# Performance work log

Measured on AMD Instinct MI355X. Metric: run time of the kernel, lower is better.

The kernel has to match this reference:

```python
import jax, jax.numpy as jnp
import numpy as np

B, T, A_DIM, Z_DIM, K = 128, 80, 32, 64, 16


def setup_inputs() -> dict:
    key = jax.random.key(0)
    k1, k2, k3, k4 = jax.random.split(key, 4)
    obs = jax.random.normal(k1, (B, T, A_DIM), jnp.float32)
    alpha_logits = jax.random.normal(k2, (B, T, K), jnp.float32)
    # torch init: A = eye(z) repeated K times; small noise keeps 80-step recursion stable
    A_K = jnp.eye(Z_DIM, dtype=jnp.float32)[None] + 0.005 * jax.random.normal(k3, (K, Z_DIM, Z_DIM), jnp.float32)
    # torch init: C = 0.05 * randn
    C_K = 0.05 * jax.random.normal(k4, (K, A_DIM, Z_DIM), jnp.float32)
    return {"obs": obs, "alpha_logits": alpha_logits, "A_K": A_K, "C_K": C_K}


def _kalman(obs, A, C):
    # obs [B,T,a], A [B,T,z,z], C [B,T,a,z]
    Bq, Tq, a_dim = obs.shape
    z_dim = A.shape[-1]
    dt = obs.dtype
    Q = 0.08 * jnp.eye(z_dim, dtype=dt)
    R = 0.03 * jnp.eye(a_dim, dtype=dt)
    I = jnp.eye(z_dim, dtype=dt)

    obs_t = jnp.swapaxes(obs, 0, 1)          # [T,B,a]
    A_t = jnp.swapaxes(A, 0, 1)              # [T,B,z,z]
    C_t = jnp.swapaxes(C, 0, 1)              # [T,B,a,z]
    A_next = jnp.concatenate([A_t[1:], A_t[-1:]], axis=0)  # A[t+1]; last unused

    mu0 = jnp.zeros((Bq, z_dim), dt)
    sig0 = jnp.broadcast_to(20.0 * I, (Bq, z_dim, z_dim))

    def filt_step(carry, inp):
        mu_p, sig_p, mu_prev = carry
        At, Anx, Ct, y = inp
        CtT = jnp.swapaxes(Ct, -1, -2)
        S = Ct @ sig_p @ CtT + R                       # [B,a,a]
        Kg = sig_p @ CtT @ jnp.linalg.inv(S)            # [B,z,a]
        Amu = jnp.einsum('bij,bj->bi', At, mu_prev)     # A_t mu_{t-1}
        err = y - jnp.einsum('bij,bj->bi', Ct, Amu)
        mu_f = Amu + jnp.einsum('bij,bj->bi', Kg, err)
        sig_f = (I - Kg @ Ct) @ sig_p
        mu_pn = jnp.einsum('bij,bj->bi', Anx, mu_f)     # prediction with A_{t+1}
        sig_pn = Anx @ sig_f @ jnp.swapaxes(Anx, -1, -2) + Q
        return (mu_pn, sig_pn, mu_f), (mu_f, sig_f, mu_p, sig_p)

    _, (mu_f, sig_f, mu_p, sig_p) = jax.lax.scan(
        filt_step, (mu0, sig0, mu0), (A_t, A_next, C_t, obs_t))

    def smooth_step(carry, inp):
        mu_s, sig_s = carry
        mf, sf, Anx, mpn, spn = inp
        J = sf @ jnp.swapaxes(Anx, -1, -2) @ jnp.linalg.inv(spn)
        mu = mf + jnp.einsum('bij,bj->bi', J, mu_s - mpn)
        sig = sf + J @ (sig_s - spn) @ jnp.swapaxes(J, -1, -2)
        return (mu, sig), (mu, sig)

    init = (mu_f[-1], sig_f[-1])
    _, (mu_sm, sig_sm) = jax.lax.scan(
        smooth_step, init,
        (mu_f[:-1], sig_f[:-1], A_t[1:], mu_p[1:], sig_p[1:]),
        reverse=True)
    mu_sm = jnp.concatenate([mu_sm, mu_f[-1:]], axis=0)
    sig_sm = jnp.concatenate([sig_sm, sig_f[-1:]], axis=0)
    return jnp.swapaxes(mu_sm, 0, 1), jnp.swapaxes(sig_sm, 0, 1)  # [B,T,z], [B,T,z,z]


def reference(obs, alpha_logits, A_K, C_K):
    w = jax.nn.softmax(alpha_logits, axis=-1)                # [B,T,K]
    A = jnp.einsum('btk,kij->btij', w, A_K)                  # [B,T,z,z]
    C = jnp.einsum('btk,kij->btij', w, C_K)                  # [B,T,a,z]
    return _kalman(obs, A, C)
```

## Files before the change

kernel.cpp:

```cpp
#include <hip/hip_runtime.h>

#define B_ 128
#define T_ 80
#define AD 32
#define ZD 64
#define KD 16
#define S8 68
#define SC 36

__device__ __forceinline__ float4 ld4(const float* p) { return *(const float4*)p; }
__device__ __forceinline__ void st4f(float* p, float4 v) { *(float4*)p = v; }

__device__ __forceinline__ float4 comb4(float4 c, float4 x0, float4 x1, float4 x2, float4 x3) {
    return make_float4(c.x*x0.x + c.y*x1.x + c.z*x2.x + c.w*x3.x,
                       c.x*x0.y + c.y*x1.y + c.z*x2.y + c.w*x3.y,
                       c.x*x0.z + c.y*x1.z + c.z*x2.z + c.w*x3.z,
                       c.x*x0.w + c.y*x1.w + c.z*x2.w + c.w*x3.w);
}

__device__ __forceinline__ void pinv4(float4 q0, float4 q1, float4 q2, float4 q3,
                                      float4& pi0, float4& pi1, float4& pi2, float4& pi3)
{
    const float ra = 1.0f / (q0.x*q1.y - q0.y*q1.x);
    const float ai00 =  q1.y*ra, ai01 = -q0.y*ra, ai10 = -q1.x*ra, ai11 = q0.x*ra;
    const float ca00 = q2.x*ai00 + q2.y*ai10, ca01 = q2.x*ai01 + q2.y*ai11;
    const float ca10 = q3.x*ai00 + q3.y*ai10, ca11 = q3.x*ai01 + q3.y*ai11;
    const float s00 = q2.z - (ca00*q0.z + ca01*q1.z), s01 = q2.w - (ca00*q0.w + ca01*q1.w);
    const float s10 = q3.z - (ca10*q0.z + ca11*q1.z), s11 = q3.w - (ca10*q0.w + ca11*q1.w);
    const float rs = 1.0f / (s00*s11 - s01*s10);
    const float si00 = s11*rs, si01 = -s01*rs, si10 = -s10*rs, si11 = s00*rs;
    const float ab00 = ai00*q0.z + ai01*q1.z, ab01 = ai00*q0.w + ai01*q1.w;
    const float ab10 = ai10*q0.z + ai11*q1.z, ab11 = ai10*q0.w + ai11*q1.w;
    const float t00 = ab00*si00 + ab01*si10, t01 = ab00*si01 + ab01*si11;
    const float t10 = ab10*si00 + ab11*si10, t11 = ab10*si01 + ab11*si11;
    const float tl00 = ai00 + (t00*ca00 + t01*ca10), tl01 = ai01 + (t00*ca01 + t01*ca11);
    const float tl10 = ai10 + (t10*ca00 + t11*ca10), tl11 = ai11 + (t10*ca01 + t11*ca11);
    const float bl00 = -(si00*ca00 + si01*ca10), bl01 = -(si00*ca01 + si01*ca11);
    const float bl10 = -(si10*ca00 + si11*ca10), bl11 = -(si10*ca01 + si11*ca11);
    pi0 = make_float4(tl00, tl01, -t00, -t01);
    pi1 = make_float4(tl10, tl11, -t10, -t11);
    pi2 = make_float4(bl00, bl01, si00, si01);
    pi3 = make_float4(bl10, bl11, si10, si11);
}

template<int KL, int AS, int BS, bool ATRANS>
__device__ __forceinline__ void mm64(const float* __restrict__ Pa, const float* __restrict__ Qb,
                                     float acc[2][4], int r2, int c4)
{
#pragma unroll 8
    for (int k = 0; k < KL; k++) {
        float aA, aB;
        if (ATRANS) { aA = Pa[k * AS + r2];   aB = Pa[k * AS + r2 + 1]; }
        else        { aA = Pa[r2 * AS + k];   aB = Pa[(r2 + 1) * AS + k]; }
        const float4 bv = ld4(&Qb[k * BS + c4]);
        acc[0][0] += aA * bv.x; acc[0][1] += aA * bv.y; acc[0][2] += aA * bv.z; acc[0][3] += aA * bv.w;
        acc[1][0] += aB * bv.x; acc[1][1] += aB * bv.y; acc[1][2] += aB * bv.z; acc[1][3] += aB * bv.w;
    }
}

__global__ __launch_bounds__(512, 2)
void kvae_kernel(const float* __restrict__ obs, const float* __restrict__ logits,
                 const float* __restrict__ AK, const float* __restrict__ CK,
                 float* __restrict__ out)
{
    __shared__ __align__(16) float W[T_ * KD];
    __shared__ __align__(16) float Am[ZD * S8];
    __shared__ __align__(16) float At[ZD * S8];
    __shared__ __align__(16) float SP[ZD * S8];
    __shared__ __align__(16) float SF[ZD * S8];
    __shared__ __align__(16) float Mm[ZD * S8];
    __shared__ __align__(16) float Pool[9984];
    __shared__ __align__(16) float pvL[512];
    __shared__ __align__(16) float pvR[512];
    __shared__ __align__(16) float fbb[512];
    __shared__ __align__(16) float pvE[8];
    __shared__ __align__(16) float y_s[32];
    __shared__ __align__(16) float errv[32];
    __shared__ __align__(16) float uev[32];
    __shared__ __align__(16) float mup[64];
    __shared__ __align__(16) float muf[64];
    __shared__ __align__(16) float mus[64];
    __shared__ __align__(16) float mpn[64];
    __shared__ __align__(16) float dv[64];

    float* T1 = Pool;
    float* CM = Pool + 2176;
    float* CT = Pool + 4352;
    float* U_ = Pool + 6656;
    float* S_ = Pool + 8832;
    float* Xb = Pool;
    float* SG = Pool + 4352;

    const int tid = threadIdx.x;
    const int b   = blockIdx.x;

    const int r16 = tid >> 4;
    const int cg  = tid & 15;
    const int c4  = cg << 2;
    const int c2  = cg << 1;
    const int r2  = r16 << 1;
    const int gi  = tid >> 3;
    const int gs  = tid & 7;

    const float* obs_b = obs    + (size_t)b * T_ * AD;
    const float* lg_b  = logits + (size_t)b * T_ * KD;
    float* omu = out + (size_t)b * T_ * ZD;
    float* osg = out + (size_t)B_ * T_ * ZD + (size_t)b * T_ * ZD * ZD;
    const float4* AK4 = (const float4*)AK;
    const float4* CK4 = (const float4*)CK;

    auto mixA = [&](int tt) {
#pragma unroll
        for (int rr = 0; rr < 2; rr++) {
            const int r = r2 + rr;
            float4 a = make_float4(0.f, 0.f, 0.f, 0.f);
#pragma unroll
            for (int k = 0; k < KD; k++) {
                const float wk = W[tt * KD + k];
                const float4 v = AK4[k * 1024 + r * 16 + cg];
                a.x += wk * v.x; a.y += wk * v.y; a.z += wk * v.z; a.w += wk * v.w;
            }
            st4f(&Am[r * S8 + c4], a);
            At[(c4 + 0) * S8 + r] = a.x; At[(c4 + 1) * S8 + r] = a.y;
            At[(c4 + 2) * S8 + r] = a.z; At[(c4 + 3) * S8 + r] = a.w;
        }
    };
    auto mixC = [&](int tt) {
        float4 a = make_float4(0.f, 0.f, 0.f, 0.f);
#pragma unroll
        for (int k = 0; k < KD; k++) {
            const float wk = W[tt * KD + k];
            const float4 v = CK4[k * 512 + r16 * 16 + cg];
            a.x += wk * v.x; a.y += wk * v.y; a.z += wk * v.z; a.w += wk * v.w;
        }
        st4f(&CM[r16 * S8 + c4], a);
        CT[(c4 + 0) * SC + r16] = a.x; CT[(c4 + 1) * SC + r16] = a.y;
        CT[(c4 + 2) * SC + r16] = a.z; CT[(c4 + 3) * SC + r16] = a.w;
    };

    if (tid < T_) {
        float l[KD]; float mx = -1e30f;
#pragma unroll
        for (int k = 0; k < KD; k++) { l[k] = lg_b[tid * KD + k]; mx = fmaxf(mx, l[k]); }
        float s = 0.f;
#pragma unroll
        for (int k = 0; k < KD; k++) { l[k] = expf(l[k] - mx); s += l[k]; }
        const float inv = 1.0f / s;
#pragma unroll
        for (int k = 0; k < KD; k++) W[tid * KD + k] = l[k] * inv;
    }
#pragma unroll
    for (int rr = 0; rr < 2; rr++) {
        const int r = r2 + rr;
#pragma unroll
        for (int j = 0; j < 4; j++) SP[r * S8 + c4 + j] = (r == c4 + j) ? 20.0f : 0.0f;
    }
    if (tid < ZD) mup[tid] = 0.0f;
    __syncthreads();

    for (int t = 0; t < T_; t++) {
        if (t < T_ - 1) mixA(t + 1);
        mixC(t);
        if (tid < AD) y_s[tid] = obs_b[t * AD + tid];
        __syncthreads();

        {
            float a0 = 0, a1 = 0, a2 = 0, a3 = 0;
            const float* pa = CM + r16 * S8;
#pragma unroll 8
            for (int k = 0; k < ZD; k++) {
                const float a = pa[k];
                const float4 bv = ld4(&SP[k * S8 + c4]);
                a0 += a * bv.x; a1 += a * bv.y; a2 += a * bv.z; a3 += a * bv.w;
            }
            T1[r16 * S8 + c4 + 0] = a0; T1[r16 * S8 + c4 + 1] = a1;
            T1[r16 * S8 + c4 + 2] = a2; T1[r16 * S8 + c4 + 3] = a3;
        }
        __syncthreads();

        {
            float a0 = 0, a1 = 0;
            const float* pa = T1 + r16 * S8;
#pragma unroll 8
            for (int k = 0; k < ZD; k++) {
                const float a = pa[k];
                const float2 bv = *(const float2*)&CT[k * SC + c2];
                a0 += a * bv.x; a1 += a * bv.y;
            }
            if (r16 == c2)     a0 += 0.03f;
            if (r16 == c2 + 1) a1 += 0.03f;
            S_[r16 * SC + c2] = a0; S_[r16 * SC + c2 + 1] = a1;
        }
        if (tid < AD) {
            float s = 0.f;
#pragma unroll
            for (int k4 = 0; k4 < ZD; k4 += 4) {
                const float4 cm = ld4(&CM[tid * S8 + k4]);
                const float4 mu = ld4(&mup[k4]);
                s += cm.x*mu.x + cm.y*mu.y + cm.z*mu.z + cm.w*mu.w;
            }
            errv[tid] = y_s[tid] - s;
        }
        __syncthreads();

        {
            const int hi = r16, hs = cg;
            float4 aL = make_float4(0, 0, 0, 0);
            float4 aR = ld4(&T1[hi * S8 + hs * 4]);
            float e = 0.f;
            if (hs < 8) aL = ld4(&S_[hi * SC + hs * 4]);
            if (hs == 15) e = errv[hi];
            if (hi < 4) {
                if (hs < 8) st4f(&pvL[hi * 32 + hs * 4], aL);
                st4f(&pvR[hi * 64 + hs * 4], aR);
                if (hs == 15) pvE[hi] = e;
            }
            if (hs == 0) st4f(&fbb[hi * 4], aL);
            __syncthreads();

#pragma unroll 2
            for (int j = 0; j < 8; ++j) {
                const int par = j & 1, nb = par ^ 1;
                const bool isp = (hi >> 2) == j;
                const float4 f  = ld4(&fbb[par * 128 + hi * 4]);
                const float4 q0 = ld4(&fbb[par * 128 + (4 * j + 0) * 4]);
                const float4 q1 = ld4(&fbb[par * 128 + (4 * j + 1) * 4]);
                const float4 q2 = ld4(&fbb[par * 128 + (4 * j + 2) * 4]);
                const float4 q3 = ld4(&fbb[par * 128 + (4 * j + 3) * 4]);
                float4 pi0, pi1, pi2, pi3;
                pinv4(q0, q1, q2, q3, pi0, pi1, pi2, pi3);
                const int rr = hi & 3;
                const float4 coef = isp ? (rr == 0 ? pi0 : rr == 1 ? pi1 : rr == 2 ? pi2 : pi3)
                                        : comb4(f, pi0, pi1, pi2, pi3);
                {
                    const float4 x0 = ld4(&pvR[par * 256 + 0 * 64 + hs * 4]);
                    const float4 x1 = ld4(&pvR[par * 256 + 1 * 64 + hs * 4]);
                    const float4 x2 = ld4(&pvR[par * 256 + 2 * 64 + hs * 4]);
                    const float4 x3 = ld4(&pvR[par * 256 + 3 * 64 + hs * 4]);
                    const float4 c = comb4(coef, x0, x1, x2, x3);
                    if (isp) aR = c;
                    else { aR.x -= c.x; aR.y -= c.y; aR.z -= c.z; aR.w -= c.w; }
                }
                if (hs < 8) {
                    const float4 x0 = ld4(&pvL[par * 128 + 0 * 32 + hs * 4]);
                    const float4 x1 = ld4(&pvL[par * 128 + 1 * 32 + hs * 4]);
                    const float4 x2 = ld4(&pvL[par * 128 + 2 * 32 + hs * 4]);
                    const float4 x3 = ld4(&pvL[par * 128 + 3 * 32 + hs * 4]);
                    const float4 c = comb4(coef, x0, x1, x2, x3);
                    if (isp) aL = c;
                    else { aL.x -= c.x; aL.y -= c.y; aL.z -= c.z; aL.w -= c.w; }
                }
                if (hs == 15) {
                    const float e0 = pvE[par * 4 + 0], e1 = pvE[par * 4 + 1];
                    const float e2 = pvE[par * 4 + 2], e3 = pvE[par * 4 + 3];
                    const float ce = coef.x * e0 + coef.y * e1 + coef.z * e2 + coef.w * e3;
                    if (isp) e = ce; else e -= ce;
                }
                if (j < 7) {
                    if ((hi >> 2) == j + 1) {
                        if (hs < 8) st4f(&pvL[nb * 128 + (hi & 3) * 32 + hs * 4], aL);
                        st4f(&pvR[nb * 256 + (hi & 3) * 64 + hs * 4], aR);
                        if (hs == 15) pvE[nb * 4 + (hi & 3)] = e;
                    }
                    if (hs == j + 1) st4f(&fbb[nb * 128 + hi * 4], aL);
                }
                __syncthreads();
            }
            st4f(&U_[hi * S8 + hs * 4], aR);
            if (hs == 15) uev[hi] = e;
        }
        __syncthreads();

        {
            float acc[2][4] = {};
            mm64<AD, S8, S8, true>(T1, U_, acc, r2, c4);
            float* og = osg + (size_t)t * ZD * ZD;
#pragma unroll
            for (int rr = 0; rr < 2; rr++) {
                const int r = r2 + rr;
                const float4 sp = ld4(&SP[r * S8 + c4]);
                const float4 v = make_float4(sp.x - acc[rr][0], sp.y - acc[rr][1],
                                             sp.z - acc[rr][2], sp.w - acc[rr][3]);
                st4f(&SF[r * S8 + c4], v);
                *(float4*)(og + r * ZD + c4) = v;
            }
        }
        if (tid < ZD) {
            float s = 0.f;
#pragma unroll
            for (int k = 0; k < AD; k++) s += T1[k * S8 + tid] * uev[k];
            const float v = mup[tid] + s;
            muf[tid] = v;
            omu[t * ZD + tid] = v;
        }
        __syncthreads();

        if (t < T_ - 1) {
            {
                float acc[2][4] = {};
                mm64<ZD, S8, S8, false>(Am, SF, acc, r2, c4);
#pragma unroll
                for (int rr = 0; rr < 2; rr++)
                    st4f(&Mm[(r2 + rr) * S8 + c4],
                         make_float4(acc[rr][0], acc[rr][1], acc[rr][2], acc[rr][3]));
            }
            __syncthreads();
            {
                float acc[2][4] = {};
                mm64<ZD, S8, S8, false>(Mm, At, acc, r2, c4);
#pragma unroll
                for (int rr = 0; rr < 2; rr++) {
                    const int r = r2 + rr;
#pragma unroll
                    for (int j = 0; j < 4; j++)
                        SP[r * S8 + c4 + j] = acc[rr][j] + ((r == c4 + j) ? 0.08f : 0.0f);
                }
            }
            if (tid >= 448) {
                const int i = tid - 448;
                float s = 0.f;
                const float* pa = Am + i * S8;
#pragma unroll 8
                for (int k = 0; k < ZD; k++) s += pa[k] * muf[k];
                mup[i] = s;
            }
            __syncthreads();
        }
    }

#pragma unroll
    for (int rr = 0; rr < 2; rr++)
        st4f(&SG[(r2 + rr) * S8 + c4], ld4(&SF[(r2 + rr) * S8 + c4]));
    if (tid < ZD) mus[tid] = muf[tid];
    __syncthreads();

    for (int t = T_ - 2; t >= 0; t--) {
        mixA(t + 1);
        {
            const float4* og4 = (const float4*)(osg + (size_t)t * ZD * ZD);
#pragma unroll
            for (int rr = 0; rr < 2; rr++)
                st4f(&SF[(r2 + rr) * S8 + c4], og4[(r2 + rr) * 16 + cg]);
        }
        if (tid >= 448) muf[tid - 448] = omu[t * ZD + (tid - 448)];
        __syncthreads();

        {
            float acc[2][4] = {};
            mm64<ZD, S8, S8, false>(Am, SF, acc, r2, c4);
#pragma unroll
            for (int rr = 0; rr < 2; rr++)
                st4f(&Mm[(r2 + rr) * S8 + c4],
                     make_float4(acc[rr][0], acc[rr][1], acc[rr][2], acc[rr][3]));
        }
        if (tid >= 448) {
            const int i = tid - 448;
            float s = 0.f;
            const float* pa = Am + i * S8;
#pragma unroll 8
            for (int k = 0; k < ZD; k++) s += pa[k] * muf[k];
            mpn[i] = s;
        }
        __syncthreads();

        {
            float acc[2][4] = {};
            mm64<ZD, S8, S8, false>(Mm, At, acc, r2, c4);
#pragma unroll
            for (int rr = 0; rr < 2; rr++) {
                const int r = r2 + rr;
#pragma unroll
                for (int j = 0; j < 4; j++)
                    SP[r * S8 + c4 + j] = acc[rr][j] + ((r == c4 + j) ? 0.08f : 0.0f);
            }
        }
        if (tid >= 448) { const int i = tid - 448; dv[i] = mus[i] - mpn[i]; }
        __syncthreads();

        {
            float4 aL0 = ld4(&SP[gi * S8 + gs * 8]);
            float4 aL1 = ld4(&SP[gi * S8 + gs * 8 + 4]);
            float4 aR0 = ld4(&Mm[gi * S8 + gs * 8]);
            float4 aR1 = ld4(&Mm[gi * S8 + gs * 8 + 4]);
            if (gi < 4) {
                st4f(&pvL[gi * 64 + gs * 8], aL0); st4f(&pvL[gi * 64 + gs * 8 + 4], aL1);
                st4f(&pvR[gi * 64 + gs * 8], aR0); st4f(&pvR[gi * 64 + gs * 8 + 4], aR1);
            }
            if (gs == 0) st4f(&fbb[gi * 4], aL0);
            __syncthreads();

#pragma unroll 2
            for (int j = 0; j < 16; ++j) {
                const int par = j & 1, nb = par ^ 1;
                const bool isp = (gi >> 2) == j;
                const float4 f  = ld4(&fbb[par * 256 + gi * 4]);
                const float4 q0 = ld4(&fbb[par * 256 + (4 * j + 0) * 4]);
                const float4 q1 = ld4(&fbb[par * 256 + (4 * j + 1) * 4]);
                const float4 q2 = ld4(&fbb[par * 256 + (4 * j + 2) * 4]);
                const float4 q3 = ld4(&fbb[par * 256 + (4 * j + 3) * 4]);
                float4 pi0, pi1, pi2, pi3;
                pinv4(q0, q1, q2, q3, pi0, pi1, pi2, pi3);
                const int rr = gi & 3;
                const float4 coef = isp ? (rr == 0 ? pi0 : rr == 1 ? pi1 : rr == 2 ? pi2 : pi3)
                                        : comb4(f, pi0, pi1, pi2, pi3);
                {
                    const float4 x0 = ld4(&pvL[par * 256 + 0 * 64 + gs * 8]);
                    const float4 x1 = ld4(&pvL[par * 256 + 1 * 64 + gs * 8]);
                    const float4 x2 = ld4(&pvL[par * 256 + 2 * 64 + gs * 8]);
                    const float4 x3 = ld4(&pvL[par * 256 + 3 * 64 + gs * 8]);
                    const float4 c = comb4(coef, x0, x1, x2, x3);
                    if (isp) aL0 = c;
                    else { aL0.x -= c.x; aL0.y -= c.y; aL0.z -= c.z; aL0.w -= c.w; }
                }
                {
                    const float4 x0 = ld4(&pvL[par * 256 + 0 * 64 + gs * 8 + 4]);
                    const float4 x1 = ld4(&pvL[par * 256 + 1 * 64 + gs * 8 + 4]);
                    const float4 x2 = ld4(&pvL[par * 256 + 2 * 64 + gs * 8 + 4]);
                    const float4 x3 = ld4(&pvL[par * 256 + 3 * 64 + gs * 8 + 4]);
                    const float4 c = comb4(coef, x0, x1, x2, x3);
                    if (isp) aL1 = c;
                    else { aL1.x -= c.x; aL1.y -= c.y; aL1.z -= c.z; aL1.w -= c.w; }
                }
                {
                    const float4 x0 = ld4(&pvR[par * 256 + 0 * 64 + gs * 8]);
                    const float4 x1 = ld4(&pvR[par * 256 + 1 * 64 + gs * 8]);
                    const float4 x2 = ld4(&pvR[par * 256 + 2 * 64 + gs * 8]);
                    const float4 x3 = ld4(&pvR[par * 256 + 3 * 64 + gs * 8]);
                    const float4 c = comb4(coef, x0, x1, x2, x3);
                    if (isp) aR0 = c;
                    else { aR0.x -= c.x; aR0.y -= c.y; aR0.z -= c.z; aR0.w -= c.w; }
                }
                {
                    const float4 x0 = ld4(&pvR[par * 256 + 0 * 64 + gs * 8 + 4]);
                    const float4 x1 = ld4(&pvR[par * 256 + 1 * 64 + gs * 8 + 4]);
                    const float4 x2 = ld4(&pvR[par * 256 + 2 * 64 + gs * 8 + 4]);
                    const float4 x3 = ld4(&pvR[par * 256 + 3 * 64 + gs * 8 + 4]);
                    const float4 c = comb4(coef, x0, x1, x2, x3);
                    if (isp) aR1 = c;
                    else { aR1.x -= c.x; aR1.y -= c.y; aR1.z -= c.z; aR1.w -= c.w; }
                }
                if (j < 15) {
                    if ((gi >> 2) == j + 1) {
                        const int rn = gi & 3;
                        st4f(&pvL[nb * 256 + rn * 64 + gs * 8], aL0);
                        st4f(&pvL[nb * 256 + rn * 64 + gs * 8 + 4], aL1);
                        st4f(&pvR[nb * 256 + rn * 64 + gs * 8], aR0);
                        st4f(&pvR[nb * 256 + rn * 64 + gs * 8 + 4], aR1);
                    }
                    if (gs == ((j + 1) >> 1))
                        st4f(&fbb[nb * 256 + gi * 4], ((j + 1) & 1) ? aL1 : aL0);
                }
                __syncthreads();
            }
            st4f(&Xb[gi * S8 + gs * 8], aR0);
            st4f(&Xb[gi * S8 + gs * 8 + 4], aR1);
        }
        __syncthreads();

        {
            float acc[2][4] = {};
            mm64<ZD, S8, S8, false>(SG, Xb, acc, r2, c4);
#pragma unroll
            for (int rr = 0; rr < 2; rr++) {
                const int r = r2 + rr;
                const float4 m = ld4(&Mm[r * S8 + c4]);
                SP[r * S8 + c4 + 0] = acc[rr][0] - m.x;
                SP[r * S8 + c4 + 1] = acc[rr][1] - m.y;
                SP[r * S8 + c4 + 2] = acc[rr][2] - m.z;
                SP[r * S8 + c4 + 3] = acc[rr][3] - m.w;
            }
        }
        __syncthreads();

        {
            float acc[2][4] = {};
            mm64<ZD, S8, S8, true>(Xb, SP, acc, r2, c4);
            float* og = osg + (size_t)t * ZD * ZD;
#pragma unroll
            for (int rr = 0; rr < 2; rr++) {
                const int r = r2 + rr;
                const float4 sf = ld4(&SF[r * S8 + c4]);
                const float4 v = make_float4(sf.x + acc[rr][0], sf.y + acc[rr][1],
                                             sf.z + acc[rr][2], sf.w + acc[rr][3]);
                st4f(&SG[r * S8 + c4], v);
                *(float4*)(og + r * ZD + c4) = v;
            }
        }
        if (tid < ZD) {
            float s = 0.f;
#pragma unroll 8
            for (int k = 0; k < ZD; k++) s += Xb[k * S8 + tid] * dv[k];
            const float v = muf[tid] + s;
            mus[tid] = v;
            omu[t * ZD + tid] = v;
        }
        __syncthreads();
    }
}

extern "C" void kernel_launch(void* const* d_in, const int* in_sizes, int n_in,
                              void* d_out, int out_size, void* d_ws, size_t ws_size,
                              hipStream_t stream) {
    const float* obs = (const float*)d_in[0];
    const float* lg  = (const float*)d_in[1];
    const float* AK  = (const float*)d_in[2];
    const float* CK  = (const float*)d_in[3];
    (void)d_ws; (void)ws_size; (void)in_sizes; (void)n_in; (void)out_size;
    kvae_kernel<<<dim3(B_), dim3(512), 0, stream>>>(obs, lg, AK, CK, (float*)d_out);
}
```

Before: 3.609 ms.

## Replace block 4x4 inverse with direct solve, skip eliminated columns, fuse pivot staging

The blocked Gauss-Jordan elimination used to form an explicit 4x4 inverse per pivot block and combine it with each row's factor. It now runs a direct 4x4 LU solve per thread instead. Column blocks already eliminated are skipped in the left-panel updates. The first pivot panel is written by the producing stages, which removes a barrier before each elimination loop, and the final stores move into the last iteration. Several matmuls switch to the transposed-A path so they can use float2 loads, which assumes matrices such as SG are symmetric. The costs are extra divides per thread and the risk of wrong results if those symmetry assumptions fail.

```diff
diff --git a/kernel.cpp b/kernel.cpp
--- a/kernel.cpp
+++ b/kernel.cpp
@@ -10,7 +10,9 @@
 
 __device__ __forceinline__ float4 ld4(const float* p) { return *(const float4*)p; }
 __device__ __forceinline__ void st4f(float* p, float4 v) { *(float4*)p = v; }
-
+__device__ __forceinline__ float4 sub4(float4 a, float4 b) {
+    return make_float4(a.x - b.x, a.y - b.y, a.z - b.z, a.w - b.w);
+}
 __device__ __forceinline__ float4 comb4(float4 c, float4 x0, float4 x1, float4 x2, float4 x3) {
     return make_float4(c.x*x0.x + c.y*x1.x + c.z*x2.x + c.w*x3.x,
                        c.x*x0.y + c.y*x1.y + c.z*x2.y + c.w*x3.y,
@@ -18,29 +20,38 @@
                        c.x*x0.w + c.y*x1.w + c.z*x2.w + c.w*x3.w);
 }
 
-__device__ __forceinline__ void pinv4(float4 q0, float4 q1, float4 q2, float4 q3,
-                                      float4& pi0, float4& pi1, float4& pi2, float4& pi3)
+__device__ __forceinline__ float4 solve4(float4 q0, float4 q1, float4 q2, float4 q3, float4 f)
 {
-    const float ra = 1.0f / (q0.x*q1.y - q0.y*q1.x);
-    const float ai00 =  q1.y*ra, ai01 = -q0.y*ra, ai10 = -q1.x*ra, ai11 = q0.x*ra;
-    const float ca00 = q2.x*ai00 + q2.y*ai10, ca01 = q2.x*ai01 + q2.y*ai11;
-    const float ca10 = q3.x*ai00 + q3.y*ai10, ca11 = q3.x*ai01 + q3.y*ai11;
-    const float s00 = q2.z - (ca00*q0.z + ca01*q1.z), s01 = q2.w - (ca00*q0.w + ca01*q1.w);
-    const float s10 = q3.z - (ca10*q0.z + ca11*q1.z), s11 = q3.w - (ca10*q0.w + ca11*q1.w);
-    const float rs = 1.0f / (s00*s11 - s01*s10);
-    const float si00 = s11*rs, si01 = -s01*rs, si10 = -s10*rs, si11 = s00*rs;
-    const float ab00 = ai00*q0.z + ai01*q1.z, ab01 = ai00*q0.w + ai01*q1.w;
-    const float ab10 = ai10*q0.z + ai11*q1.z, ab11 = ai10*q0.w + ai11*q1.w;
-    const float t00 = ab00*si00 + ab01*si10, t01 = ab00*si01 + ab01*si11;
-    const float t10 = ab10*si00 + ab11*si10, t11 = ab10*si01 + ab11*si11;
-    const float tl00 = ai00 + (t00*ca00 + t01*ca10), tl01 = ai01 + (t00*ca01 + t01*ca11);
-    const float tl10 = ai10 + (t10*ca00 + t11*ca10), tl11 = ai11 + (t10*ca01 + t11*ca11);
-    const float bl00 = -(si00*ca00 + si01*ca10), bl01 = -(si00*ca01 + si01*ca11);
-    const float bl10 = -(si10*ca00 + si11*ca10), bl11 = -(si10*ca01 + si11*ca11);
-    pi0 = make_float4(tl00, tl01, -t00, -t01);
-    pi1 = make_float4(tl10, tl11, -t10, -t11);
-    pi2 = make_float4(bl00, bl01, si00, si01);
-    pi3 = make_float4(bl10, bl11, si10, si11);
+    float a01 = q1.x, a02 = q2.x, a03 = q3.x, b0 = f.x;
+    float a11 = q1.y, a12 = q2.y, a13 = q3.y, b1 = f.y;
+    float a21 = q1.z, a22 = q2.z, a23 = q3.z, b2 = f.z;
+    float a31 = q1.w, a32 = q2.w, a33 = q3.w, b3 = f.w;
+    const float r0 = 1.0f / q0.x;
+    {
+        const float m1 = q0.y * r0;
+        a11 -= m1*a01; a12 -= m1*a02; a13 -= m1*a03; b1 -= m1*b0;
+        const float m2 = q0.z * r0;
+        a21 -= m2*a01; a22 -= m2*a02; a23 -= m2*a03; b2 -= m2*b0;
+        const float m3 = q0.w * r0;
+        a31 -= m3*a01; a32 -= m3*a02; a33 -= m3*a03; b3 -= m3*b0;
+    }
+    const float r1 = 1.0f / a11;
+    {
+        const float m2 = a21 * r1;
+        a22 -= m2*a12; a23 -= m2*a13; b2 -= m2*b1;
+        const float m3 = a31 * r1;
+        a32 -= m3*a12; a33 -= m3*a13; b3 -= m3*b1;
+    }
+    const float r2 = 1.0f / a22;
+    {
+        const float m3 = a32 * r2;
+        a33 -= m3*a23; b3 -= m3*b2;
+    }
+    const float x3 = b3 / a33;
+    const float x2 = (b2 - a23*x3) * r2;
+    const float x1 = (b1 - a13*x3 - a12*x2) * r1;
+    const float x0 = (b0 - a03*x3 - a02*x2 - a01*x1) * r0;
+    return make_float4(x0, x1, x2, x3);
 }
 
 template<int KL, int AS, int BS, bool ATRANS>
@@ -50,8 +61,12 @@
 #pragma unroll 8
     for (int k = 0; k < KL; k++) {
         float aA, aB;
-        if (ATRANS) { aA = Pa[k * AS + r2];   aB = Pa[k * AS + r2 + 1]; }
-        else        { aA = Pa[r2 * AS + k];   aB = Pa[(r2 + 1) * AS + k]; }
+        if (ATRANS) {
+            const float2 av = *(const float2*)&Pa[k * AS + r2];
+            aA = av.x; aB = av.y;
+        } else {
+            aA = Pa[r2 * AS + k]; aB = Pa[(r2 + 1) * AS + k];
+        }
         const float4 bv = ld4(&Qb[k * BS + c4]);
         acc[0][0] += aA * bv.x; acc[0][1] += aA * bv.y; acc[0][2] += aA * bv.z; acc[0][3] += aA * bv.w;
         acc[1][0] += aB * bv.x; acc[1][1] += aB * bv.y; acc[1][2] += aB * bv.z; acc[1][3] += aB * bv.w;
@@ -190,6 +205,8 @@
             if (r16 == c2)     a0 += 0.03f;
             if (r16 == c2 + 1) a1 += 0.03f;
             S_[r16 * SC + c2] = a0; S_[r16 * SC + c2 + 1] = a1;
+            if (c2 < 4) { fbb[r16 * 4 + c2] = a0; fbb[r16 * 4 + c2 + 1] = a1; }
+            if (r16 < 4) { pvL[r16 * 32 + c2] = a0; pvL[r16 * 32 + c2 + 1] = a1; }
         }
         if (tid < AD) {
             float s = 0.f;
@@ -199,7 +216,13 @@
                 const float4 mu = ld4(&mup[k4]);
                 s += cm.x*mu.x + cm.y*mu.y + cm.z*mu.z + cm.w*mu.w;
             }
-            errv[tid] = y_s[tid] - s;
+            const float e_ = y_s[tid] - s;
+            errv[tid] = e_;
+            if (tid < 4) pvE[tid] = e_;
+        }
+        if (tid >= 448) {
+            const int u = tid - 448; const int rr = u >> 4, cc = (u & 15) << 2;
+            st4f(&pvR[rr * 64 + cc], ld4(&T1[rr * S8 + cc]));
         }
         __syncthreads();
 
@@ -210,66 +233,55 @@
             float e = 0.f;
             if (hs < 8) aL = ld4(&S_[hi * SC + hs * 4]);
             if (hs == 15) e = errv[hi];
-            if (hi < 4) {
-                if (hs < 8) st4f(&pvL[hi * 32 + hs * 4], aL);
-                st4f(&pvR[hi * 64 + hs * 4], aR);
-                if (hs == 15) pvE[hi] = e;
-            }
-            if (hs == 0) st4f(&fbb[hi * 4], aL);
-            __syncthreads();
 
 #pragma unroll 2
             for (int j = 0; j < 8; ++j) {
                 const int par = j & 1, nb = par ^ 1;
                 const bool isp = (hi >> 2) == j;
-                const float4 f  = ld4(&fbb[par * 128 + hi * 4]);
+                const int i4 = hi & 3;
                 const float4 q0 = ld4(&fbb[par * 128 + (4 * j + 0) * 4]);
                 const float4 q1 = ld4(&fbb[par * 128 + (4 * j + 1) * 4]);
                 const float4 q2 = ld4(&fbb[par * 128 + (4 * j + 2) * 4]);
                 const float4 q3 = ld4(&fbb[par * 128 + (4 * j + 3) * 4]);
-                float4 pi0, pi1, pi2, pi3;
-                pinv4(q0, q1, q2, q3, pi0, pi1, pi2, pi3);
-                const int rr = hi & 3;
-                const float4 coef = isp ? (rr == 0 ? pi0 : rr == 1 ? pi1 : rr == 2 ? pi2 : pi3)
-                                        : comb4(f, pi0, pi1, pi2, pi3);
+                float4 f;
+                if (isp) f = make_float4(i4 == 0, i4 == 1, i4 == 2, i4 == 3);
+                else     f = ld4(&fbb[par * 128 + hi * 4]);
+                const float4 coef = solve4(q0, q1, q2, q3, f);
                 {
-                    const float4 x0 = ld4(&pvR[par * 256 + 0 * 64 + hs * 4]);
-                    const float4 x1 = ld4(&pvR[par * 256 + 1 * 64 + hs * 4]);
-                    const float4 x2 = ld4(&pvR[par * 256 + 2 * 64 + hs * 4]);
-                    const float4 x3 = ld4(&pvR[par * 256 + 3 * 64 + hs * 4]);
-                    const float4 c = comb4(coef, x0, x1, x2, x3);
-                    if (isp) aR = c;
-                    else { aR.x -= c.x; aR.y -= c.y; aR.z -= c.z; aR.w -= c.w; }
-                }
-                if (hs < 8) {
-                    const float4 x0 = ld4(&pvL[par * 128 + 0 * 32 + hs * 4]);
-                    const float4 x1 = ld4(&pvL[par * 128 + 1 * 32 + hs * 4]);
-                    const float4 x2 = ld4(&pvL[par * 128 + 2 * 32 + hs * 4]);
-                    const float4 x3 = ld4(&pvL[par * 128 + 3 * 32 + hs * 4]);
-                    const float4 c = comb4(coef, x0, x1, x2, x3);
-                    if (isp) aL = c;
-                    else { aL.x -= c.x; aL.y -= c.y; aL.z -= c.z; aL.w -= c.w; }
+                    const float4 c = comb4(coef,
+                        ld4(&pvR[par * 256 + 0 * 64 + hs * 4]),
+                        ld4(&pvR[par * 256 + 1 * 64 + hs * 4]),
+                        ld4(&pvR[par * 256 + 2 * 64 + hs * 4]),
+                        ld4(&pvR[par * 256 + 3 * 64 + hs * 4]));
+                    if (isp) aR = c; else aR = sub4(aR, c);
+                }
+                if (hs < 8 && hs >= j) {
+                    const float4 c = comb4(coef,
+                        ld4(&pvL[par * 128 + 0 * 32 + hs * 4]),
+                        ld4(&pvL[par * 128 + 1 * 32 + hs * 4]),
+                        ld4(&pvL[par * 128 + 2 * 32 + hs * 4]),
+                        ld4(&pvL[par * 128 + 3 * 32 + hs * 4]));
+                    if (isp) aL = c; else aL = sub4(aL, c);
                 }
                 if (hs == 15) {
-                    const float e0 = pvE[par * 4 + 0], e1 = pvE[par * 4 + 1];
-                    const float e2 = pvE[par * 4 + 2], e3 = pvE[par * 4 + 3];
-                    const float ce = coef.x * e0 + coef.y * e1 + coef.z * e2 + coef.w * e3;
+                    const float4 ev = ld4(&pvE[par * 4]);
+                    const float ce = coef.x*ev.x + coef.y*ev.y + coef.z*ev.z + coef.w*ev.w;
                     if (isp) e = ce; else e -= ce;
                 }
                 if (j < 7) {
                     if ((hi >> 2) == j + 1) {
-                        if (hs < 8) st4f(&pvL[nb * 128 + (hi & 3) * 32 + hs * 4], aL);
-                        st4f(&pvR[nb * 256 + (hi & 3) * 64 + hs * 4], aR);
-                        if (hs == 15) pvE[nb * 4 + (hi & 3)] = e;
+                        if (hs < 8 && hs >= j) st4f(&pvL[nb * 128 + i4 * 32 + hs * 4], aL);
+                        st4f(&pvR[nb * 256 + i4 * 64 + hs * 4], aR);
+                        if (hs == 15) pvE[nb * 4 + i4] = e;
                     }
                     if (hs == j + 1) st4f(&fbb[nb * 128 + hi * 4], aL);
+                } else {
+                    st4f(&U_[hi * S8 + hs * 4], aR);
+                    if (hs == 15) uev[hi] = e;
                 }
                 __syncthreads();
             }
-            st4f(&U_[hi * S8 + hs * 4], aR);
-            if (hs == 15) uev[hi] = e;
-        }
-        __syncthreads();
+        }
 
         {
             float acc[2][4] = {};
@@ -298,7 +310,7 @@
         if (t < T_ - 1) {
             {
                 float acc[2][4] = {};
-                mm64<ZD, S8, S8, false>(Am, SF, acc, r2, c4);
+                mm64<ZD, S8, S8, true>(At, SF, acc, r2, c4);
 #pragma unroll
                 for (int rr = 0; rr < 2; rr++)
                     st4f(&Mm[(r2 + rr) * S8 + c4],
@@ -347,7 +359,7 @@
 
         {
             float acc[2][4] = {};
-            mm64<ZD, S8, S8, false>(Am, SF, acc, r2, c4);
+            mm64<ZD, S8, S8, true>(At, SF, acc, r2, c4);
 #pragma unroll
             for (int rr = 0; rr < 2; rr++)
                 st4f(&Mm[(r2 + rr) * S8 + c4],
@@ -366,15 +378,27 @@
         {
             float acc[2][4] = {};
             mm64<ZD, S8, S8, false>(Mm, At, acc, r2, c4);
-#pragma unroll
-            for (int rr = 0; rr < 2; rr++) {
-                const int r = r2 + rr;
-#pragma unroll
-                for (int j = 0; j < 4; j++)
-                    SP[r * S8 + c4 + j] = acc[rr][j] + ((r == c4 + j) ? 0.08f : 0.0f);
+            float4 v0 = make_float4(acc[0][0] + ((r2 == c4 + 0) ? 0.08f : 0.0f),
+                                    acc[0][1] + ((r2 == c4 + 1) ? 0.08f : 0.0f),
+                                    acc[0][2] + ((r2 == c4 + 2) ? 0.08f : 0.0f),
+                                    acc[0][3] + ((r2 == c4 + 3) ? 0.08f : 0.0f));
+            float4 v1 = make_float4(acc[1][0] + ((r2 + 1 == c4 + 0) ? 0.08f : 0.0f),
+                                    acc[1][1] + ((r2 + 1 == c4 + 1) ? 0.08f : 0.0f),
+                                    acc[1][2] + ((r2 + 1 == c4 + 2) ? 0.08f : 0.0f),
+                                    acc[1][3] + ((r2 + 1 == c4 + 3) ? 0.08f : 0.0f));
+            st4f(&SP[r2 * S8 + c4], v0);
+            st4f(&SP[(r2 + 1) * S8 + c4], v1);
+            if (c4 == 0) { st4f(&fbb[r2 * 4], v0); st4f(&fbb[(r2 + 1) * 4], v1); }
+            if (r2 < 4) {
+                st4f(&pvL[r2 * 64 + c4], v0);
+                st4f(&pvL[(r2 + 1) * 64 + c4], v1);
             }
         }
         if (tid >= 448) { const int i = tid - 448; dv[i] = mus[i] - mpn[i]; }
+        if (tid < 64) {
+            const int rr = tid >> 4, cc = (tid & 15) << 2;
+            st4f(&pvR[rr * 64 + cc], ld4(&Mm[rr * S8 + cc]));
+        }
         __syncthreads();
 
         {
@@ -382,84 +406,70 @@
             float4 aL1 = ld4(&SP[gi * S8 + gs * 8 + 4]);
             float4 aR0 = ld4(&Mm[gi * S8 + gs * 8]);
             float4 aR1 = ld4(&Mm[gi * S8 + gs * 8 + 4]);
-            if (gi < 4) {
-                st4f(&pvL[gi * 64 + gs * 8], aL0); st4f(&pvL[gi * 64 + gs * 8 + 4], aL1);
-                st4f(&pvR[gi * 64 + gs * 8], aR0); st4f(&pvR[gi * 64 + gs * 8 + 4], aR1);
-            }
-            if (gs == 0) st4f(&fbb[gi * 4], aL0);
-            __syncthreads();
 
 #pragma unroll 2
             for (int j = 0; j < 16; ++j) {
                 const int par = j & 1, nb = par ^ 1;
                 const bool isp = (gi >> 2) == j;
-                const float4 f  = ld4(&fbb[par * 256 + gi * 4]);
+                const int i4 = gi & 3;
                 const float4 q0 = ld4(&fbb[par * 256 + (4 * j + 0) * 4]);
                 const float4 q1 = ld4(&fbb[par * 256 + (4 * j + 1) * 4]);
                 const float4 q2 = ld4(&fbb[par * 256 + (4 * j + 2) * 4]);
                 const float4 q3 = ld4(&fbb[par * 256 + (4 * j + 3) * 4]);
-                float4 pi0, pi1, pi2, pi3;
-                pinv4(q0, q1, q2, q3, pi0, pi1, pi2, pi3);
-                const int rr = gi & 3;
-                const float4 coef = isp ? (rr == 0 ? pi0 : rr == 1 ? pi1 : rr == 2 ? pi2 : pi3)
-                                        : comb4(f, pi0, pi1, pi2, pi3);
+                float4 f;
+                if (isp) f = make_float4(i4 == 0, i4 == 1, i4 == 2, i4 == 3);
+                else     f = ld4(&fbb[par * 256 + gi * 4]);
+                const float4 coef = solve4(q0, q1, q2, q3, f);
                 {
-                    const float4 x0 = ld4(&pvL[par * 256 + 0 * 64 + gs * 8]);
-                    const float4 x1 = ld4(&pvL[par * 256 + 1 * 64 + gs * 8]);
-                    const float4 x2 = ld4(&pvL[par * 256 + 2 * 64 + gs * 8]);
-                    const float4 x3 = ld4(&pvL[par * 256 + 3 * 64 + gs * 8]);
-                    const float4 c = comb4(coef, x0, x1, x2, x3);
-                    if (isp) aL0 = c;
-                    else { aL0.x -= c.x; aL0.y -= c.y; aL0.z -= c.z; aL0.w -= c.w; }
-                }
-                {
-                    const float4 x0 = ld4(&pvL[par * 256 + 0 * 64 + gs * 8 + 4]);
-                    const float4 x1 = ld4(&pvL[par * 256 + 1 * 64 + gs * 8 + 4]);
-                    const float4 x2 = ld4(&pvL[par * 256 + 2 * 64 + gs * 8 + 4]);
-                    const float4 x3 = ld4(&pvL[par * 256 + 3 * 64 + gs * 8 + 4]);
-                    const float4 c = comb4(coef, x0, x1, x2, x3);
-                    if (isp) aL1 = c;
-                    else { aL1.x -= c.x; aL1.y -= c.y; aL1.z -= c.z; aL1.w -= c.w; }
-                }
-                {
-                    const float4 x0 = ld4(&pvR[par * 256 + 0 * 64 + gs * 8]);
-                    const float4 x1 = ld4(&pvR[par * 256 + 1 * 64 + gs * 8]);
-                    const float4 x2 = ld4(&pvR[par * 256 + 2 * 64 + gs * 8]);
-                    const float4 x3 = ld4(&pvR[par * 256 + 3 * 64 + gs * 8]);
-                    const float4 c = comb4(coef, x0, x1, x2, x3);
-                    if (isp) aR0 = c;
-                    else { aR0.x -= c.x; aR0.y -= c.y; aR0.z -= c.z; aR0.w -= c.w; }
-                }
-                {
-                    const float4 x0 = ld4(&pvR[par * 256 + 0 * 64 + gs * 8 + 4]);
-                    const float4 x1 = ld4(&pvR[par * 256 + 1 * 64 + gs * 8 + 4]);
-                    const float4 x2 = ld4(&pvR[par * 256 + 2 * 64 + gs * 8 + 4]);
-                    const float4 x3 = ld4(&pvR[par * 256 + 3 * 64 + gs * 8 + 4]);
-                    const float4 c = comb4(coef, x0, x1, x2, x3);
-                    if (isp) aR1 = c;
-                    else { aR1.x -= c.x; aR1.y -= c.y; aR1.z -= c.z; aR1.w -= c.w; }
+                    const float4 c0 = comb4(coef,
+                        ld4(&pvR[par * 256 + 0 * 64 + gs * 8]),
+                        ld4(&pvR[par * 256 + 1 * 64 + gs * 8]),
+                        ld4(&pvR[par * 256 + 2 * 64 + gs * 8]),
+                        ld4(&pvR[par * 256 + 3 * 64 + gs * 8]));
+                    const float4 c1 = comb4(coef,
+                        ld4(&pvR[par * 256 + 0 * 64 + gs * 8 + 4]),
+                        ld4(&pvR[par * 256 + 1 * 64 + gs * 8 + 4]),
+                        ld4(&pvR[par * 256 + 2 * 64 + gs * 8 + 4]),
+                        ld4(&pvR[par * 256 + 3 * 64 + gs * 8 + 4]));
+                    if (isp) { aR0 = c0; aR1 = c1; }
+                    else     { aR0 = sub4(aR0, c0); aR1 = sub4(aR1, c1); }
+                }
+                if (2 * gs >= j) {
+                    const float4 c0 = comb4(coef,
+                        ld4(&pvL[par * 256 + 0 * 64 + gs * 8]),
+                        ld4(&pvL[par * 256 + 1 * 64 + gs * 8]),
+                        ld4(&pvL[par * 256 + 2 * 64 + gs * 8]),
+                        ld4(&pvL[par * 256 + 3 * 64 + gs * 8]));
+                    if (isp) aL0 = c0; else aL0 = sub4(aL0, c0);
+                }
+                if (2 * gs + 1 >= j) {
+                    const float4 c1 = comb4(coef,
+                        ld4(&pvL[par * 256 + 0 * 64 + gs * 8 + 4]),
+                        ld4(&pvL[par * 256 + 1 * 64 + gs * 8 + 4]),
+                        ld4(&pvL[par * 256 + 2 * 64 + gs * 8 + 4]),
+                        ld4(&pvL[par * 256 + 3 * 64 + gs * 8 + 4]));
+                    if (isp) aL1 = c1; else aL1 = sub4(aL1, c1);
                 }
                 if (j < 15) {
                     if ((gi >> 2) == j + 1) {
-                        const int rn = gi & 3;
-                        st4f(&pvL[nb * 256 + rn * 64 + gs * 8], aL0);
-                        st4f(&pvL[nb * 256 + rn * 64 + gs * 8 + 4], aL1);
-                        st4f(&pvR[nb * 256 + rn * 64 + gs * 8], aR0);
-                        st4f(&pvR[nb * 256 + rn * 64 + gs * 8 + 4], aR1);
+                        st4f(&pvR[nb * 256 + i4 * 64 + gs * 8], aR0);
+                        st4f(&pvR[nb * 256 + i4 * 64 + gs * 8 + 4], aR1);
+                        if (2 * gs >= j)     st4f(&pvL[nb * 256 + i4 * 64 + gs * 8], aL0);
+                        if (2 * gs + 1 >= j) st4f(&pvL[nb * 256 + i4 * 64 + gs * 8 + 4], aL1);
                     }
                     if (gs == ((j + 1) >> 1))
                         st4f(&fbb[nb * 256 + gi * 4], ((j + 1) & 1) ? aL1 : aL0);
+                } else {
+                    st4f(&Xb[gi * S8 + gs * 8], aR0);
+                    st4f(&Xb[gi * S8 + gs * 8 + 4], aR1);
                 }
                 __syncthreads();
             }
-            st4f(&Xb[gi * S8 + gs * 8], aR0);
-            st4f(&Xb[gi * S8 + gs * 8 + 4], aR1);
-        }
-        __syncthreads();
+        }
 
         {
             float acc[2][4] = {};
-            mm64<ZD, S8, S8, false>(SG, Xb, acc, r2, c4);
+            mm64<ZD, S8, S8, true>(SG, Xb, acc, r2, c4);
 #pragma unroll
             for (int rr = 0; rr < 2; rr++) {
                 const int r = r2 + rr;
```

Result: slower. 3.950 ms (+9.4%).
